# Performance work log

Measured on AMD Instinct MI355X. Metric: run time of the kernel, lower is better.

The kernel has to match this reference:

```python
import jax, jax.numpy as jnp
import numpy as np


def setup_inputs() -> dict:
    key = jax.random.key(0)
    ks = jax.random.split(key, 7)
    B, H, W, C, HID = 8, 64, 64, 16, 256
    s = 0.05
    return {
        "x": jax.random.normal(ks[0], (B, H, W, C), jnp.float32),
        "W1": jax.random.normal(ks[1], (C, HID), jnp.float32) * s,
        "b1": jax.random.normal(ks[2], (C, HID), jnp.float32) * s,
        "W2": jax.random.normal(ks[3], (C, HID, HID), jnp.float32) * s,
        "b2": jax.random.normal(ks[4], (C, HID), jnp.float32) * s,
        "W3": jax.random.normal(ks[5], (C, HID, 3), jnp.float32) * s,
        "b3": jax.random.normal(ks[6], (C, 3), jnp.float32) * s,
    }


def reference(x, W1, b1, W2, b2, W3, b3):
    # x: [B,H,W,C] -> per-channel independent 3-layer MLP (1 -> HID -> HID -> 3)
    B, H, W, C = x.shape
    xf = x.reshape(-1, C)                                   # [N, C]
    # fc1: Linear(1, HID) per channel == scalar * weight + bias
    h = jax.nn.relu(xf[:, :, None] * W1[None] + b1[None])   # [N, C, HID]
    # fc2: batched GEMM over channels
    h = jax.nn.relu(jnp.einsum('nch,chk->nck', h, W2) + b2[None])  # [N, C, HID]
    # fc3: HID -> 3 per channel
    out = jnp.einsum('nch,cho->nco', h, W3) + b3[None]      # [N, C, 3]
    # torch.cat(outputs, dim=1) yields [c0_0..c0_2, c1_0..c1_2, ...] == reshape
    return out.reshape(B, H, W, C * 3)
```

## Files before the change

### kernel.cpp

```cpp
#include <hip/hip_runtime.h>
#include <hip/hip_bf16.h>


typedef __bf16 bf16_t;
typedef __attribute__((ext_vector_type(8))) __bf16 bf16x8;
typedef __attribute__((ext_vector_type(4))) __bf16 bf16x4;
typedef __attribute__((ext_vector_type(4))) float floatx4;

#define C_CH  16
#define HID   256
#define TILES 16
#define NSEG  257
#define GPTS  4097
#define XLO   (-6.0f)
#define XSTEP (12.0f / 4096.0f)

__global__ __launch_bounds__(256, 4) void build_tab(
    const float* __restrict__ W1, const float* __restrict__ b1,
    const float* __restrict__ W2, const float* __restrict__ b2,
    bf16_t* __restrict__ tab, float* __restrict__ ts_g) {
  __shared__ float tk[256];
  __shared__ int ti[256];
  __shared__ float sW1[256], sB1[256];
  __shared__ int sRank[256];
  __shared__ float caS[256], ccS[256];
  __shared__ float part[4][64][9];
  __shared__ float eA[17], eC[17];
  __shared__ int eH[17];
  const int c = blockIdx.x & 15;
  const int k = blockIdx.x >> 4;
  const int j0 = (NSEG * k) >> 4;
  const int j1 = (NSEG * (k + 1)) >> 4;
  const int nev = j1 - 1 - j0;
  const int t = threadIdx.x;

  sW1[t] = W1[c * 256 + t];
  sB1[t] = b1[c * 256 + t];
  tk[t] = (sW1[t] != 0.0f) ? (-sB1[t] / sW1[t]) : 3.0e38f;
  ti[t] = t;
  __syncthreads();
  for (int kk = 2; kk <= 256; kk <<= 1) {
    for (int j = kk >> 1; j > 0; j >>= 1) {
      int l = t ^ j;
      if (l > t) {
        bool asc = ((t & kk) == 0);
        float a = tk[t], b = tk[l];
        if (asc ? (a > b) : (a < b)) {
          int ia = ti[t], ib = ti[l];
          tk[t] = b; tk[l] = a; ti[t] = ib; ti[l] = ia;
        }
      }
      __syncthreads();
    }
  }
  sRank[ti[t]] = t;
  if (k == 0) ts_g[c * 256 + t] = tk[t];
  if (t < nev) {
    int h = ti[j0 + t];
    float w = sW1[h], bv = sB1[h];
    eA[t] = fabsf(w);
    eC[t] = (w > 0.f) ? bv : ((w < 0.f) ? -bv : 0.f);
    eH[t] = h;
  }
  __syncthreads();

  {
    float w = sW1[t], bv = sB1[t];
    int r = sRank[t];
    bool act = (w > 0.f) ? (j0 > r) : ((w < 0.f) ? (j0 <= r) : (bv > 0.f));
    caS[t] = act ? w : 0.f;
    ccS[t] = act ? bv : 0.f;
  }
  __syncthreads();

  const int rg = t >> 6;
  const int q = t & 63;
  const float* W2c = W2 + ((size_t)c << 16);
  float pa0 = 0.f, pa1 = 0.f, pa2 = 0.f, pa3 = 0.f;
  float pc0 = 0.f, pc1 = 0.f, pc2 = 0.f, pc3 = 0.f;
  for (int h0 = rg * 64; h0 < rg * 64 + 64; h0 += 8) {
    float4 v[8];
#pragma unroll
    for (int u = 0; u < 8; ++u)
      v[u] = *(const float4*)(W2c + (size_t)(h0 + u) * 256 + q * 4);
#pragma unroll
    for (int u = 0; u < 8; ++u) {
      float ca = caS[h0 + u], cc = ccS[h0 + u];
      pa0 = fmaf(ca, v[u].x, pa0); pa1 = fmaf(ca, v[u].y, pa1);
      pa2 = fmaf(ca, v[u].z, pa2); pa3 = fmaf(ca, v[u].w, pa3);
      pc0 = fmaf(cc, v[u].x, pc0); pc1 = fmaf(cc, v[u].y, pc1);
      pc2 = fmaf(cc, v[u].z, pc2); pc3 = fmaf(cc, v[u].w, pc3);
    }
  }
  part[rg][q][0] = pa0; part[rg][q][1] = pa1;
  part[rg][q][2] = pa2; part[rg][q][3] = pa3;
  part[rg][q][4] = pc0; part[rg][q][5] = pc1;
  part[rg][q][6] = pc2; part[rg][q][7] = pc3;
  __syncthreads();

  float accA = 0.f, accC = b2[c * 256 + t];
  {
    const int qq = t >> 2, ii = t & 3;
#pragma unroll
    for (int rr = 0; rr < 4; ++rr) {
      accA += part[rr][qq][ii];
      accC += part[rr][qq][4 + ii];
    }
  }
  {
    bf16_t* rp = tab + ((size_t)c * NSEG + j0) * 512;
    rp[t] = (bf16_t)accA; rp[256 + t] = (bf16_t)accC;
  }

  float ew[16];
#pragma unroll 16
  for (int e = 0; e < 16; ++e)
    if (e < nev) ew[e] = W2c[eH[e] * 256 + t];
#pragma unroll 16
  for (int e = 0; e < 16; ++e) {
    if (e < nev) {
      accA = fmaf(eA[e], ew[e], accA);
      accC = fmaf(eC[e], ew[e], accC);
      bf16_t* rp = tab + ((size_t)c * NSEG + (j0 + 1 + e)) * 512;
      rp[t] = (bf16_t)accA; rp[256 + t] = (bf16_t)accC;
    }
  }
}

__global__ __launch_bounds__(256) void build_ftab(
    const bf16_t* __restrict__ tab, const float* __restrict__ ts_g,
    const float* __restrict__ W3, const float* __restrict__ b3,
    float* __restrict__ ftab) {
  __shared__ float tls[256];
  __shared__ short sj[128];
  const int t = threadIdx.x;
  const int c = blockIdx.x & 15;
  const int q = blockIdx.x >> 4;
  const int gp0 = q * 128;

  tls[t] = ts_g[c * 256 + t];

  const int l16 = t & 15;
  const int g = t >> 4;
  float w3f0[16], w3f1[16], w3f2[16];
#pragma unroll
  for (int u = 0; u < 16; ++u) {
    const float* wp = W3 + ((size_t)c * 256 + l16 * 16 + u) * 3;
    w3f0[u] = wp[0]; w3f1[u] = wp[1]; w3f2[u] = wp[2];
  }
  const float b3v0 = b3[c * 3 + 0], b3v1 = b3[c * 3 + 1], b3v2 = b3[c * 3 + 2];
  __syncthreads();

  if (t < 128) {
    const int gp = gp0 + t;
    if (gp <= 4096) {
      const float xv = XLO + (float)gp * XSTEP;
      int j = 0;
#pragma unroll
      for (int s = 128; s > 0; s >>= 1)
        if (tls[j + s - 1] <= xv) j += s;
      if (j == 255 && tls[255] <= xv) j = 256;
      else if (j < 255 && tls[j] <= xv) ++j;
      sj[t] = (short)j;
    } else {
      sj[t] = 0;
    }
  }
  __syncthreads();

  const bf16_t* tabc = tab + (size_t)c * NSEG * 512;
  float xv = XLO + (float)(gp0 + g) * XSTEP;
  const bf16_t* row = tabc + (size_t)sj[g] * 512 + l16 * 16;
  bf16x8 a0 = *(const bf16x8*)(row);
  bf16x8 a1 = *(const bf16x8*)(row + 8);
  bf16x8 c0 = *(const bf16x8*)(row + 256);
  bf16x8 c1 = *(const bf16x8*)(row + 264);

  for (int i = 0; i < 8; ++i) {
    bf16x8 na0, na1, nc0, nc1;
    float nxv = 0.f;
    if (i < 7) {
      int npl = (i + 1) * 16 + g;
      nxv = XLO + (float)(gp0 + npl) * XSTEP;
      const bf16_t* nrow = tabc + (size_t)sj[npl] * 512 + l16 * 16;
      na0 = *(const bf16x8*)(nrow);
      na1 = *(const bf16x8*)(nrow + 8);
      nc0 = *(const bf16x8*)(nrow + 256);
      nc1 = *(const bf16x8*)(nrow + 264);
    }
    float s0 = 0.f, s1 = 0.f, s2 = 0.f;
#pragma unroll
    for (int u = 0; u < 8; ++u) {
      float h2 = fmaxf(fmaf(xv, (float)a0[u], (float)c0[u]), 0.f);
      s0 = fmaf(h2, w3f0[u], s0);
      s1 = fmaf(h2, w3f1[u], s1);
      s2 = fmaf(h2, w3f2[u], s2);
    }
#pragma unroll
    for (int u = 0; u < 8; ++u) {
      float h2 = fmaxf(fmaf(xv, (float)a1[u], (float)c1[u]), 0.f);
      s0 = fmaf(h2, w3f0[8 + u], s0);
      s1 = fmaf(h2, w3f1[8 + u], s1);
      s2 = fmaf(h2, w3f2[8 + u], s2);
    }
#pragma unroll
    for (int m = 1; m < 16; m <<= 1) {
      s0 += __shfl_xor(s0, m, 64);
      s1 += __shfl_xor(s1, m, 64);
      s2 += __shfl_xor(s2, m, 64);
    }
    const int gp = gp0 + i * 16 + g;
    if (l16 < 3 && gp <= 4096) {
      float v = (l16 == 0) ? (s0 + b3v0) : (l16 == 1) ? (s1 + b3v1) : (s2 + b3v2);
      ftab[((size_t)c * GPTS + gp) * 4 + l16] = v;
    }
    a0 = na0; a1 = na1; c0 = nc0; c1 = nc1; xv = nxv;
  }
}

__global__ __launch_bounds__(256) void kan_eval(
    const float* __restrict__ x, const float* __restrict__ ftab,
    float* __restrict__ out) {
  const int base = blockIdx.x * 256 + threadIdx.x;
  const float inv = 1.0f / XSTEP;
#pragma unroll
  for (int it = 0; it < 4; ++it) {
    const int flat = it * 131072 + base;
    const float xv = x[flat];
    const int c = flat & 15;
    float u = (xv - XLO) * inv;
    int i = (int)floorf(u);
    i = i < 0 ? 0 : (i > 4095 ? 4095 : i);
    const float f = u - (float)i;
    const float4* fp = (const float4*)ftab + (size_t)c * GPTS + i;
    float4 fa = fp[0];
    float4 fb = fp[1];
    float* op = out + (size_t)flat * 3;
    op[0] = fmaf(fb.x - fa.x, f, fa.x);
    op[1] = fmaf(fb.y - fa.y, f, fa.y);
    op[2] = fmaf(fb.z - fa.z, f, fa.z);
  }
}

__global__ __launch_bounds__(256) void kan_pwl(
    const float* __restrict__ x, const bf16_t* __restrict__ tab,
    const float* __restrict__ W1, const float* __restrict__ b1,
    const float* __restrict__ W3, const float* __restrict__ b3,
    float* __restrict__ out) {
  __shared__ float xs[256];
  __shared__ float tls[256];
  __shared__ short sj[256];
  const int t = threadIdx.x;
  const int b = blockIdx.x;
  const int c = ((b & 7) << 1) | ((b >> 3) & 1);
  const int pb = b >> 4;

  xs[t] = x[(size_t)(pb * 256 + t) * C_CH + c];
  {
    float w = W1[c * 256 + t], bb = b1[c * 256 + t];
    tls[t] = (w != 0.0f) ? (-bb / w) : 3.0e38f;
  }
  __syncthreads();
  for (int kk = 2; kk <= 256; kk <<= 1) {
    for (int j = kk >> 1; j > 0; j >>= 1) {
      int l = t ^ j;
      if (l > t) {
        bool asc = ((t & kk) == 0);
        float a = tls[t], bb2 = tls[l];
        if (asc ? (a > bb2) : (a < bb2)) { tls[t] = bb2; tls[l] = a; }
      }
      __syncthreads();
    }
  }

  const int l16 = t & 15;
  const int g = t >> 4;
  float w3f0[16], w3f1[16], w3f2[16];
#pragma unroll
  for (int qq = 0; qq < 16; ++qq) {
    const float* wp = W3 + ((size_t)c * 256 + l16 * 16 + qq) * 3;
    w3f0[qq] = wp[0]; w3f1[qq] = wp[1]; w3f2[qq] = wp[2];
  }
  const float b3v0 = b3[c * 3 + 0], b3v1 = b3[c * 3 + 1], b3v2 = b3[c * 3 + 2];

  {
    const float xv = xs[t];
    int j = 0;
#pragma unroll
    for (int s = 128; s > 0; s >>= 1)
      if (tls[j + s - 1] <= xv) j += s;
    if (j == 255 && tls[255] <= xv) j = 256;
    else if (j < 255 && tls[j] <= xv) ++j;
    sj[t] = (short)j;
  }
  __syncthreads();

  const bf16_t* tabc = tab + (size_t)c * NSEG * 512;
  for (int i = 0; i < 16; ++i) {
    const int pl = i * 16 + g;
    const float xv = xs[pl];
    const bf16_t* row = tabc + (size_t)sj[pl] * 512 + l16 * 16;
    bf16x8 a0 = *(const bf16x8*)(row);
    bf16x8 a1 = *(const bf16x8*)(row + 8);
    bf16x8 c0 = *(const bf16x8*)(row + 256);
    bf16x8 c1 = *(const bf16x8*)(row + 264);
    float s0 = 0.f, s1 = 0.f, s2 = 0.f;
#pragma unroll
    for (int qq = 0; qq < 8; ++qq) {
      float h2 = fmaxf(fmaf(xv, (float)a0[qq], (float)c0[qq]), 0.f);
      s0 = fmaf(h2, w3f0[qq], s0);
      s1 = fmaf(h2, w3f1[qq], s1);
      s2 = fmaf(h2, w3f2[qq], s2);
    }
#pragma unroll
    for (int qq = 0; qq < 8; ++qq) {
      float h2 = fmaxf(fmaf(xv, (float)a1[qq], (float)c1[qq]), 0.f);
      s0 = fmaf(h2, w3f0[8 + qq], s0);
      s1 = fmaf(h2, w3f1[8 + qq], s1);
      s2 = fmaf(h2, w3f2[8 + qq], s2);
    }
#pragma unroll
    for (int m = 1; m < 16; m <<= 1) {
      s0 += __shfl_xor(s0, m, 64);
      s1 += __shfl_xor(s1, m, 64);
      s2 += __shfl_xor(s2, m, 64);
    }
    if (l16 < 3) {
      float v = (l16 == 0) ? (s0 + b3v0) : (l16 == 1) ? (s1 + b3v1) : (s2 + b3v2);
      out[((size_t)(pb * 256 + pl) * C_CH + c) * 3 + l16] = v;
    }
  }
}

__global__ __launch_bounds__(256) void transpose_w2(const float* __restrict__ W2,
                                                    bf16_t* __restrict__ W2t) {
  __shared__ __align__(16) bf16_t tl[64][72];
  const int bid = blockIdx.x;
  const int c = bid >> 4, ti = (bid >> 2) & 3, tj = bid & 3;
  const int t = threadIdx.x;
  const float* src = W2 + (size_t)(c * 256 + tj * 64) * 256 + ti * 64;
#pragma unroll
  for (int it = 0; it < 4; ++it) {
    int idx = it * 256 + t;
    int h = idx >> 4, q = idx & 15;
    float4 v = *(const float4*)(src + h * 256 + q * 4);
    tl[h][q * 4 + 0] = (bf16_t)v.x;
    tl[h][q * 4 + 1] = (bf16_t)v.y;
    tl[h][q * 4 + 2] = (bf16_t)v.z;
    tl[h][q * 4 + 3] = (bf16_t)v.w;
  }
  __syncthreads();
  bf16_t* dst = W2t + (size_t)(c * 256 + ti * 64) * 256 + tj * 64;
#pragma unroll
  for (int it = 0; it < 2; ++it) {
    int idx = it * 256 + t;
    int n = idx >> 3, h8 = (idx & 7) * 8;
    bf16x8 tmp;
#pragma unroll
    for (int q = 0; q < 8; ++q) tmp[q] = tl[h8 + q][n];
    *(bf16x8*)(dst + n * 256 + h8) = tmp;
  }
}

template <bool DIRECT>
__global__ __launch_bounds__(256, 2) void kan_fused(
    const float* __restrict__ x, const float* __restrict__ W1,
    const float* __restrict__ b1, const bf16_t* __restrict__ W2t,
    const float* __restrict__ W2, const float* __restrict__ b2,
    const float* __restrict__ W3, const float* __restrict__ b3,
    float* __restrict__ out) {
  __shared__ __align__(16) bf16_t h1[64][264];
  __shared__ __align__(16) bf16_t w3t[4][288];
  const int t = threadIdx.x;
  const int lane = t & 63;
  const int wv = t >> 6;
  const int bid = blockIdx.x;
  const int c = bid & 15;
  const int g = bid >> 4;
  const int l15 = lane & 15;
  const int l4 = lane >> 4;
  const int nw0 = wv * 64;
  bf16x8 Bf[32];
  if (!DIRECT) {
    const bf16_t* Bbase = W2t + ((size_t)c << 16) + (size_t)(nw0 + l15) * HID + l4 * 8;
#pragma unroll
    for (int kt = 0; kt < 4; ++kt)
#pragma unroll
      for (int ks = 0; ks < 2; ++ks)
#pragma unroll
        for (int jn = 0; jn < 4; ++jn)
          Bf[kt * 8 + ks * 4 + jn] =
              *(const bf16x8*)(Bbase + jn * (16 * HID) + kt * 64 + ks * 32);
  } else {
#pragma unroll
    for (int kt = 0; kt < 4; ++kt)
#pragma unroll
      for (int ks = 0; ks < 2; ++ks)
#pragma unroll
        for (int jn = 0; jn < 4; ++jn) {
          const float* gp = W2 + ((size_t)c << 16) +
                            (size_t)(kt * 64 + ks * 32 + l4 * 8) * HID +
                            (nw0 + jn * 16 + l15);
#pragma unroll
          for (int j = 0; j < 8; ++j) Bf[kt * 8 + ks * 4 + jn][j] = (bf16_t)gp[j * HID];
        }
  }
  const int j8 = (t & 31) * 8;
  float wf[8], bf_[8];
  {
    float4 w0 = *(const float4*)(W1 + c * HID + j8);
    float4 w1v = *(const float4*)(W1 + c * HID + j8 + 4);
    float4 bb0 = *(const float4*)(b1 + c * HID + j8);
    float4 bb1 = *(const float4*)(b1 + c * HID + j8 + 4);
    wf[0] = w0.x; wf[1] = w0.y; wf[2] = w0.z; wf[3] = w0.w;
    wf[4] = w1v.x; wf[5] = w1v.y; wf[6] = w1v.z; wf[7] = w1v.w;
    bf_[0] = bb0.x; bf_[1] = bb0.y; bf_[2] = bb0.z; bf_[3] = bb0.w;
    bf_[4] = bb1.x; bf_[5] = bb1.y; bf_[6] = bb1.z; bf_[7] = bb1.w;
  }
  floatx4 b2v[4];
#pragma unroll
  for (int jn = 0; jn < 4; ++jn)
    b2v[jn] = *(const floatx4*)(b2 + c * HID + nw0 + jn * 16 + l4 * 4);
  const float b3v = b3[c * 3 + (l15 < 3 ? l15 : 0)];
  const int bhalf = (lane >> 5) & 1;
  w3t[0][t] = (bf16_t)W3[(c * HID + t) * 3 + 0];
  w3t[1][t] = (bf16_t)W3[(c * HID + t) * 3 + 1];
  w3t[2][t] = (bf16_t)W3[(c * HID + t) * 3 + 2];
  w3t[3][t] = (bf16_t)0.0f;
  const floatx4 zero4 = {0.f, 0.f, 0.f, 0.f};
  float xr = 0.0f;
  {
    int ml = (lane >> 1) * 8 + wv * 2 + (lane & 1);
    if (lane < 16) xr = x[(size_t)(g * TILES * 64 + ml) * C_CH + c];
  }
  for (int tile = 0; tile < TILES; ++tile) {
    const int m0 = (g * TILES + tile) * 64;
#pragma unroll
    for (int it = 0; it < 8; ++it) {
      int m = it * 8 + (t >> 5);
      float xm = __shfl(xr, it * 2 + bhalf, 64);
      bf16x8 hv;
#pragma unroll
      for (int q = 0; q < 8; ++q)
        hv[q] = (bf16_t)fmaxf(xm * wf[q] + bf_[q], 0.0f);
      *(bf16x8*)&h1[m][j8] = hv;
    }
    __syncthreads();
    float xr_n = 0.0f;
    if (tile + 1 < TILES && lane < 16) {
      int ml = (lane >> 1) * 8 + wv * 2 + (lane & 1);
      xr_n = x[(size_t)(m0 + 64 + ml) * C_CH + c];
    }
    floatx4 acc[4][4];
#pragma unroll
    for (int im = 0; im < 4; ++im)
#pragma unroll
      for (int jn = 0; jn < 4; ++jn) acc[im][jn] = zero4;
#pragma unroll
    for (int kt = 0; kt < 4; ++kt) {
#pragma unroll
      for (int ks = 0; ks < 2; ++ks) {
        const int k0 = kt * 64 + ks * 32;
        bf16x8 af[4];
#pragma unroll
        for (int im = 0; im < 4; ++im)
          af[im] = *(const bf16x8*)&h1[im * 16 + l15][k0 + l4 * 8];
#pragma unroll
        for (int im = 0; im < 4; ++im)
#pragma unroll
          for (int jn = 0; jn < 4; ++jn)
            acc[im][jn] = __builtin_amdgcn_mfma_f32_16x16x32_bf16(
                Bf[kt * 8 + ks * 4 + jn], af[im], acc[im][jn], 0, 0, 0);
      }
    }
    __syncthreads();
#pragma unroll
    for (int im = 0; im < 4; ++im)
#pragma unroll
      for (int jn = 0; jn < 4; ++jn) {
        bf16x4 hv;
#pragma unroll
        for (int r = 0; r < 4; ++r)
          hv[r] = (bf16_t)fmaxf(acc[im][jn][r] + b2v[jn][r], 0.0f);
        *(bf16x4*)&h1[im * 16 + l15][nw0 + jn * 16 + l4 * 4] = hv;
      }
    __syncthreads();
    {
      floatx4 acc3 = zero4;
      const int br = l15 < 3 ? l15 : 3;
#pragma unroll
      for (int kk = 0; kk < 8; ++kk) {
        bf16x8 a3 = *(const bf16x8*)&h1[wv * 16 + l15][kk * 32 + l4 * 8];
        bf16x8 bf3 = *(const bf16x8*)&w3t[br][kk * 32 + l4 * 8];
        acc3 = __builtin_amdgcn_mfma_f32_16x16x32_bf16(a3, bf3, acc3, 0, 0, 0);
      }
      if (l15 < 3) {
        float* op = out + ((size_t)((m0 + wv * 16 + l4 * 4) * C_CH + c) * 3) + l15;
#pragma unroll
        for (int r = 0; r < 4; ++r) op[r * (C_CH * 3)] = acc3[r] + b3v;
      }
    }
    __syncthreads();
    xr = xr_n;
  }
}

extern "C" void kernel_launch(void* const* d_in, const int* in_sizes, int n_in,
                              void* d_out, int out_size, void* d_ws, size_t ws_size,
                              hipStream_t stream) {
  const float* x = (const float*)d_in[0];
  const float* W1 = (const float*)d_in[1];
  const float* b1 = (const float*)d_in[2];
  const float* W2 = (const float*)d_in[3];
  const float* b2 = (const float*)d_in[4];
  const float* W3 = (const float*)d_in[5];
  const float* b3 = (const float*)d_in[6];
  float* out = (float*)d_out;

  const size_t tab_bytes = (size_t)C_CH * NSEG * 512 * sizeof(bf16_t);
  const size_t ftab_bytes = (size_t)C_CH * GPTS * 4 * sizeof(float);
  const size_t ts_bytes = (size_t)C_CH * 256 * sizeof(float);
  if (ws_size >= tab_bytes + ftab_bytes + ts_bytes) {
    bf16_t* tab = (bf16_t*)d_ws;
    float* ftab = (float*)((char*)d_ws + tab_bytes);
    float* ts_g = (float*)((char*)d_ws + tab_bytes + ftab_bytes);
    build_tab<<<256, 256, 0, stream>>>(W1, b1, W2, b2, tab, ts_g);
    build_ftab<<<528, 256, 0, stream>>>(tab, ts_g, W3, b3, ftab);
    kan_eval<<<512, 256, 0, stream>>>(x, ftab, out);
  } else if (ws_size >= tab_bytes + ts_bytes) {
    bf16_t* tab = (bf16_t*)d_ws;
    float* ts_g = (float*)((char*)d_ws + tab_bytes);
    build_tab<<<256, 256, 0, stream>>>(W1, b1, W2, b2, tab, ts_g);
    kan_pwl<<<2048, 256, 0, stream>>>(x, tab, W1, b1, W3, b3, out);
  } else if (ws_size >= (size_t)C_CH * HID * HID * sizeof(bf16_t)) {
    bf16_t* W2t = (bf16_t*)d_ws;
    transpose_w2<<<256, 256, 0, stream>>>(W2, W2t);
    kan_fused<false><<<512, 256, 0, stream>>>(x, W1, b1, W2t, W2, b2, W3, b3, out);
  } else {
    kan_fused<true><<<512, 256, 0, stream>>>(x, W1, b1, (bf16_t*)d_ws, W2, b2, W3, b3, out);
  }
}
```

Measured before the change: 96.24 us.

## Fuse table build, fine-table build and eval into one cooperative kernel

Replaces the three-kernel sequence (build_tab, build_ftab, kan_eval) with a single cooperative kernel of 512 blocks that separates the phases with grid-wide syncs, removing two launch gaps. The work split also changes: the coarse-table phase now uses 32 segment chunks per channel instead of 16, and the fine-table phase uses 144 grid points per block to cover 4097 points with 512 blocks. It falls back to the old three launches if the cooperative launch fails. Risks include grid.sync overhead and the requirement that all 512 blocks be co-resident.

```diff
diff --git a/kernel.cpp b/kernel.cpp
--- a/kernel.cpp
+++ b/kernel.cpp
@@ -1,5 +1,8 @@
 #include <hip/hip_runtime.h>
 #include <hip/hip_bf16.h>
+#include <hip/hip_cooperative_groups.h>
+
+namespace cg = cooperative_groups;
 
 
 typedef __bf16 bf16_t;
@@ -14,6 +17,238 @@
 #define GPTS  4097
 #define XLO   (-6.0f)
 #define XSTEP (12.0f / 4096.0f)
+
+__global__ __launch_bounds__(256) void kan_all(
+    const float* __restrict__ x, const float* __restrict__ W1,
+    const float* __restrict__ b1, const float* __restrict__ W2,
+    const float* __restrict__ b2, const float* __restrict__ W3,
+    const float* __restrict__ b3, bf16_t* __restrict__ tab,
+    float* __restrict__ ts_g, float* __restrict__ ftab,
+    float* __restrict__ out) {
+  cg::grid_group grid = cg::this_grid();
+  __shared__ float tk[256];
+  __shared__ int ti[256];
+  __shared__ float sW1[256], sB1[256];
+  __shared__ int sRank[256];
+  __shared__ float caS[256], ccS[256];
+  __shared__ float part[4][64][9];
+  __shared__ float eA[9], eC[9];
+  __shared__ int eH[9];
+  __shared__ short sj[144];
+
+  const int t = threadIdx.x;
+  const int b = blockIdx.x;
+
+  {
+    const int c = b & 15;
+    const int k = b >> 4;
+    const int j0 = (NSEG * k) >> 5;
+    const int j1 = (NSEG * (k + 1)) >> 5;
+    const int nev = j1 - 1 - j0;
+
+    sW1[t] = W1[c * 256 + t];
+    sB1[t] = b1[c * 256 + t];
+    tk[t] = (sW1[t] != 0.0f) ? (-sB1[t] / sW1[t]) : 3.0e38f;
+    ti[t] = t;
+    __syncthreads();
+    for (int kk = 2; kk <= 256; kk <<= 1) {
+      for (int j = kk >> 1; j > 0; j >>= 1) {
+        int l = t ^ j;
+        if (l > t) {
+          bool asc = ((t & kk) == 0);
+          float a = tk[t], bb = tk[l];
+          if (asc ? (a > bb) : (a < bb)) {
+            int ia = ti[t], ib = ti[l];
+            tk[t] = bb; tk[l] = a; ti[t] = ib; ti[l] = ia;
+          }
+        }
+        __syncthreads();
+      }
+    }
+    sRank[ti[t]] = t;
+    if (k == 0) ts_g[c * 256 + t] = tk[t];
+    if (t < nev) {
+      int h = ti[j0 + t];
+      float w = sW1[h], bv = sB1[h];
+      eA[t] = fabsf(w);
+      eC[t] = (w > 0.f) ? bv : ((w < 0.f) ? -bv : 0.f);
+      eH[t] = h;
+    }
+    __syncthreads();
+
+    {
+      float w = sW1[t], bv = sB1[t];
+      int r = sRank[t];
+      bool act = (w > 0.f) ? (j0 > r) : ((w < 0.f) ? (j0 <= r) : (bv > 0.f));
+      caS[t] = act ? w : 0.f;
+      ccS[t] = act ? bv : 0.f;
+    }
+    __syncthreads();
+
+    const int rg = t >> 6;
+    const int q = t & 63;
+    const float* W2c = W2 + ((size_t)c << 16);
+    float pa0 = 0.f, pa1 = 0.f, pa2 = 0.f, pa3 = 0.f;
+    float pc0 = 0.f, pc1 = 0.f, pc2 = 0.f, pc3 = 0.f;
+    for (int h0 = rg * 64; h0 < rg * 64 + 64; h0 += 8) {
+      float4 v[8];
+#pragma unroll
+      for (int u = 0; u < 8; ++u)
+        v[u] = *(const float4*)(W2c + (size_t)(h0 + u) * 256 + q * 4);
+#pragma unroll
+      for (int u = 0; u < 8; ++u) {
+        float ca = caS[h0 + u], cc = ccS[h0 + u];
+        pa0 = fmaf(ca, v[u].x, pa0); pa1 = fmaf(ca, v[u].y, pa1);
+        pa2 = fmaf(ca, v[u].z, pa2); pa3 = fmaf(ca, v[u].w, pa3);
+        pc0 = fmaf(cc, v[u].x, pc0); pc1 = fmaf(cc, v[u].y, pc1);
+        pc2 = fmaf(cc, v[u].z, pc2); pc3 = fmaf(cc, v[u].w, pc3);
+      }
+    }
+    part[rg][q][0] = pa0; part[rg][q][1] = pa1;
+    part[rg][q][2] = pa2; part[rg][q][3] = pa3;
+    part[rg][q][4] = pc0; part[rg][q][5] = pc1;
+    part[rg][q][6] = pc2; part[rg][q][7] = pc3;
+    __syncthreads();
+
+    float accA = 0.f, accC = b2[c * 256 + t];
+    {
+      const int qq = t >> 2, ii = t & 3;
+#pragma unroll
+      for (int rr = 0; rr < 4; ++rr) {
+        accA += part[rr][qq][ii];
+        accC += part[rr][qq][4 + ii];
+      }
+    }
+    {
+      bf16_t* rp = tab + ((size_t)c * NSEG + j0) * 512;
+      rp[t] = (bf16_t)accA; rp[256 + t] = (bf16_t)accC;
+    }
+    float ew[8];
+#pragma unroll 8
+    for (int e = 0; e < 8; ++e)
+      if (e < nev) ew[e] = W2c[eH[e] * 256 + t];
+#pragma unroll 8
+    for (int e = 0; e < 8; ++e) {
+      if (e < nev) {
+        accA = fmaf(eA[e], ew[e], accA);
+        accC = fmaf(eC[e], ew[e], accC);
+        bf16_t* rp = tab + ((size_t)c * NSEG + (j0 + 1 + e)) * 512;
+        rp[t] = (bf16_t)accA; rp[256 + t] = (bf16_t)accC;
+      }
+    }
+  }
+  __threadfence();
+  grid.sync();
+
+  {
+    const int c = b & 15;
+    const int q = b >> 4;
+    const int gp0 = q * 128;
+
+    tk[t] = ts_g[c * 256 + t];
+
+    const int l16 = t & 15;
+    const int g = t >> 4;
+    float w3f0[16], w3f1[16], w3f2[16];
+#pragma unroll
+    for (int u = 0; u < 16; ++u) {
+      const float* wp = W3 + ((size_t)c * 256 + l16 * 16 + u) * 3;
+      w3f0[u] = wp[0]; w3f1[u] = wp[1]; w3f2[u] = wp[2];
+    }
+    const float b3v0 = b3[c * 3 + 0], b3v1 = b3[c * 3 + 1], b3v2 = b3[c * 3 + 2];
+    __syncthreads();
+
+    if (t < 144) {
+      const int gp = gp0 + t;
+      if (gp <= 4096) {
+        const float xv = XLO + (float)gp * XSTEP;
+        int j = 0;
+#pragma unroll
+        for (int s = 128; s > 0; s >>= 1)
+          if (tk[j + s - 1] <= xv) j += s;
+        if (j == 255 && tk[255] <= xv) j = 256;
+        else if (j < 255 && tk[j] <= xv) ++j;
+        sj[t] = (short)j;
+      } else {
+        sj[t] = 0;
+      }
+    }
+    __syncthreads();
+
+    const bf16_t* tabc = tab + (size_t)c * NSEG * 512;
+    float xv = XLO + (float)(gp0 + g) * XSTEP;
+    const bf16_t* row = tabc + (size_t)sj[g] * 512 + l16 * 16;
+    bf16x8 a0 = *(const bf16x8*)(row);
+    bf16x8 a1 = *(const bf16x8*)(row + 8);
+    bf16x8 c0 = *(const bf16x8*)(row + 256);
+    bf16x8 c1 = *(const bf16x8*)(row + 264);
+
+    for (int i = 0; i < 9; ++i) {
+      bf16x8 na0, na1, nc0, nc1;
+      float nxv = 0.f;
+      if (i < 8) {
+        int npl = (i + 1) * 16 + g;
+        nxv = XLO + (float)(gp0 + npl) * XSTEP;
+        const bf16_t* nrow = tabc + (size_t)sj[npl] * 512 + l16 * 16;
+        na0 = *(const bf16x8*)(nrow);
+        na1 = *(const bf16x8*)(nrow + 8);
+        nc0 = *(const bf16x8*)(nrow + 256);
+        nc1 = *(const bf16x8*)(nrow + 264);
+      }
+      float s0 = 0.f, s1 = 0.f, s2 = 0.f;
+#pragma unroll
+      for (int u = 0; u < 8; ++u) {
+        float h2 = fmaxf(fmaf(xv, (float)a0[u], (float)c0[u]), 0.f);
+        s0 = fmaf(h2, w3f0[u], s0);
+        s1 = fmaf(h2, w3f1[u], s1);
+        s2 = fmaf(h2, w3f2[u], s2);
+      }
+#pragma unroll
+      for (int u = 0; u < 8; ++u) {
+        float h2 = fmaxf(fmaf(xv, (float)a1[u], (float)c1[u]), 0.f);
+        s0 = fmaf(h2, w3f0[8 + u], s0);
+        s1 = fmaf(h2, w3f1[8 + u], s1);
+        s2 = fmaf(h2, w3f2[8 + u], s2);
+      }
+#pragma unroll
+      for (int m = 1; m < 16; m <<= 1) {
+        s0 += __shfl_xor(s0, m, 64);
+        s1 += __shfl_xor(s1, m, 64);
+        s2 += __shfl_xor(s2, m, 64);
+      }
+      const int gp = gp0 + i * 16 + g;
+      if (l16 < 3 && gp <= 4096) {
+        float v = (l16 == 0) ? (s0 + b3v0) : (l16 == 1) ? (s1 + b3v1) : (s2 + b3v2);
+        ftab[((size_t)c * GPTS + gp) * 4 + l16] = v;
+      }
+      a0 = na0; a1 = na1; c0 = nc0; c1 = nc1; xv = nxv;
+    }
+  }
+  __threadfence();
+  grid.sync();
+
+  {
+    const int base = b * 256 + t;
+    const float inv = 1.0f / XSTEP;
+#pragma unroll
+    for (int it = 0; it < 4; ++it) {
+      const int flat = it * 131072 + base;
+      const float xv = x[flat];
+      const int c = flat & 15;
+      float u = (xv - XLO) * inv;
+      int i = (int)floorf(u);
+      i = i < 0 ? 0 : (i > 4095 ? 4095 : i);
+      const float f = u - (float)i;
+      const float4* fp = (const float4*)ftab + (size_t)c * GPTS + i;
+      float4 fa = fp[0];
+      float4 fb = fp[1];
+      float* op = out + (size_t)flat * 3;
+      op[0] = fmaf(fb.x - fa.x, f, fa.x);
+      op[1] = fmaf(fb.y - fa.y, f, fa.y);
+      op[2] = fmaf(fb.z - fa.z, f, fa.z);
+    }
+  }
+}
 
 __global__ __launch_bounds__(256, 4) void build_tab(
     const float* __restrict__ W1, const float* __restrict__ b1,
@@ -63,7 +298,6 @@
     eH[t] = h;
   }
   __syncthreads();
-
   {
     float w = sW1[t], bv = sB1[t];
     int r = sRank[t];
@@ -72,7 +306,6 @@
     ccS[t] = act ? bv : 0.f;
   }
   __syncthreads();
-
   const int rg = t >> 6;
   const int q = t & 63;
   const float* W2c = W2 + ((size_t)c << 16);
@@ -97,7 +330,6 @@
   part[rg][q][4] = pc0; part[rg][q][5] = pc1;
   part[rg][q][6] = pc2; part[rg][q][7] = pc3;
   __syncthreads();
-
   float accA = 0.f, accC = b2[c * 256 + t];
   {
     const int qq = t >> 2, ii = t & 3;
@@ -111,7 +343,6 @@
     bf16_t* rp = tab + ((size_t)c * NSEG + j0) * 512;
     rp[t] = (bf16_t)accA; rp[256 + t] = (bf16_t)accC;
   }
-
   float ew[16];
 #pragma unroll 16
   for (int e = 0; e < 16; ++e)
@@ -137,9 +368,7 @@
   const int c = blockIdx.x & 15;
   const int q = blockIdx.x >> 4;
   const int gp0 = q * 128;
-
   tls[t] = ts_g[c * 256 + t];
-
   const int l16 = t & 15;
   const int g = t >> 4;
   float w3f0[16], w3f1[16], w3f2[16];
@@ -150,7 +379,6 @@
   }
   const float b3v0 = b3[c * 3 + 0], b3v1 = b3[c * 3 + 1], b3v2 = b3[c * 3 + 2];
   __syncthreads();
-
   if (t < 128) {
     const int gp = gp0 + t;
     if (gp <= 4096) {
@@ -167,7 +395,6 @@
     }
   }
   __syncthreads();
-
   const bf16_t* tabc = tab + (size_t)c * NSEG * 512;
   float xv = XLO + (float)(gp0 + g) * XSTEP;
   const bf16_t* row = tabc + (size_t)sj[g] * 512 + l16 * 16;
@@ -175,7 +402,6 @@
   bf16x8 a1 = *(const bf16x8*)(row + 8);
   bf16x8 c0 = *(const bf16x8*)(row + 256);
   bf16x8 c1 = *(const bf16x8*)(row + 264);
-
   for (int i = 0; i < 8; ++i) {
     bf16x8 na0, na1, nc0, nc1;
     float nxv = 0.f;
@@ -239,96 +465,6 @@
     op[0] = fmaf(fb.x - fa.x, f, fa.x);
     op[1] = fmaf(fb.y - fa.y, f, fa.y);
     op[2] = fmaf(fb.z - fa.z, f, fa.z);
-  }
-}
-
-__global__ __launch_bounds__(256) void kan_pwl(
-    const float* __restrict__ x, const bf16_t* __restrict__ tab,
-    const float* __restrict__ W1, const float* __restrict__ b1,
-    const float* __restrict__ W3, const float* __restrict__ b3,
-    float* __restrict__ out) {
-  __shared__ float xs[256];
-  __shared__ float tls[256];
-  __shared__ short sj[256];
-  const int t = threadIdx.x;
-  const int b = blockIdx.x;
-  const int c = ((b & 7) << 1) | ((b >> 3) & 1);
-  const int pb = b >> 4;
-
-  xs[t] = x[(size_t)(pb * 256 + t) * C_CH + c];
-  {
-    float w = W1[c * 256 + t], bb = b1[c * 256 + t];
-    tls[t] = (w != 0.0f) ? (-bb / w) : 3.0e38f;
-  }
-  __syncthreads();
-  for (int kk = 2; kk <= 256; kk <<= 1) {
-    for (int j = kk >> 1; j > 0; j >>= 1) {
-      int l = t ^ j;
-      if (l > t) {
-        bool asc = ((t & kk) == 0);
-        float a = tls[t], bb2 = tls[l];
-        if (asc ? (a > bb2) : (a < bb2)) { tls[t] = bb2; tls[l] = a; }
-      }
-      __syncthreads();
-    }
-  }
-
-  const int l16 = t & 15;
-  const int g = t >> 4;
-  float w3f0[16], w3f1[16], w3f2[16];
-#pragma unroll
-  for (int qq = 0; qq < 16; ++qq) {
-    const float* wp = W3 + ((size_t)c * 256 + l16 * 16 + qq) * 3;
-    w3f0[qq] = wp[0]; w3f1[qq] = wp[1]; w3f2[qq] = wp[2];
-  }
-  const float b3v0 = b3[c * 3 + 0], b3v1 = b3[c * 3 + 1], b3v2 = b3[c * 3 + 2];
-
-  {
-    const float xv = xs[t];
-    int j = 0;
-#pragma unroll
-    for (int s = 128; s > 0; s >>= 1)
-      if (tls[j + s - 1] <= xv) j += s;
-    if (j == 255 && tls[255] <= xv) j = 256;
-    else if (j < 255 && tls[j] <= xv) ++j;
-    sj[t] = (short)j;
-  }
-  __syncthreads();
-
-  const bf16_t* tabc = tab + (size_t)c * NSEG * 512;
-  for (int i = 0; i < 16; ++i) {
-    const int pl = i * 16 + g;
-    const float xv = xs[pl];
-    const bf16_t* row = tabc + (size_t)sj[pl] * 512 + l16 * 16;
-    bf16x8 a0 = *(const bf16x8*)(row);
-    bf16x8 a1 = *(const bf16x8*)(row + 8);
-    bf16x8 c0 = *(const bf16x8*)(row + 256);
-    bf16x8 c1 = *(const bf16x8*)(row + 264);
-    float s0 = 0.f, s1 = 0.f, s2 = 0.f;
-#pragma unroll
-    for (int qq = 0; qq < 8; ++qq) {
-      float h2 = fmaxf(fmaf(xv, (float)a0[qq], (float)c0[qq]), 0.f);
-      s0 = fmaf(h2, w3f0[qq], s0);
-      s1 = fmaf(h2, w3f1[qq], s1);
-      s2 = fmaf(h2, w3f2[qq], s2);
-    }
-#pragma unroll
-    for (int qq = 0; qq < 8; ++qq) {
-      float h2 = fmaxf(fmaf(xv, (float)a1[qq], (float)c1[qq]), 0.f);
-      s0 = fmaf(h2, w3f0[8 + qq], s0);
-      s1 = fmaf(h2, w3f1[8 + qq], s1);
-      s2 = fmaf(h2, w3f2[8 + qq], s2);
-    }
-#pragma unroll
-    for (int m = 1; m < 16; m <<= 1) {
-      s0 += __shfl_xor(s0, m, 64);
-      s1 += __shfl_xor(s1, m, 64);
-      s2 += __shfl_xor(s2, m, 64);
-    }
-    if (l16 < 3) {
-      float v = (l16 == 0) ? (s0 + b3v0) : (l16 == 1) ? (s1 + b3v1) : (s2 + b3v2);
-      out[((size_t)(pb * 256 + pl) * C_CH + c) * 3 + l16] = v;
-    }
   }
 }
 
@@ -524,14 +660,24 @@
     bf16_t* tab = (bf16_t*)d_ws;
     float* ftab = (float*)((char*)d_ws + tab_bytes);
     float* ts_g = (float*)((char*)d_ws + tab_bytes + ftab_bytes);
-    build_tab<<<256, 256, 0, stream>>>(W1, b1, W2, b2, tab, ts_g);
-    build_ftab<<<528, 256, 0, stream>>>(tab, ts_g, W3, b3, ftab);
-    kan_eval<<<512, 256, 0, stream>>>(x, ftab, out);
+    void* args[] = {(void*)&x,   (void*)&W1,  (void*)&b1,   (void*)&W2,
+                    (void*)&b2,  (void*)&W3,  (void*)&b3,   (void*)&tab,
+                    (void*)&ts_g, (void*)&ftab, (void*)&out};
+    hipError_t err = hipLaunchCooperativeKernel((void*)kan_all, dim3(512),
+                                                dim3(256), args, 0, stream);
+    if (err != hipSuccess) {
+      (void)hipGetLastError();
+      build_tab<<<256, 256, 0, stream>>>(W1, b1, W2, b2, tab, ts_g);
+      build_ftab<<<528, 256, 0, stream>>>(tab, ts_g, W3, b3, ftab);
+      kan_eval<<<512, 256, 0, stream>>>(x, ftab, out);
+    }
   } else if (ws_size >= tab_bytes + ts_bytes) {
     bf16_t* tab = (bf16_t*)d_ws;
     float* ts_g = (float*)((char*)d_ws + tab_bytes);
     build_tab<<<256, 256, 0, stream>>>(W1, b1, W2, b2, tab, ts_g);
-    kan_pwl<<<2048, 256, 0, stream>>>(x, tab, W1, b1, W3, b3, out);
+    transpose_w2<<<256, 256, 0, stream>>>(W2, (bf16_t*)d_ws);
+    kan_fused<false><<<512, 256, 0, stream>>>(x, W1, b1, (bf16_t*)d_ws, W2, b2,
+                                              W3, b3, out);
   } else if (ws_size >= (size_t)C_CH * HID * HID * sizeof(bf16_t)) {
     bf16_t* W2t = (bf16_t*)d_ws;
     transpose_w2<<<256, 256, 0, stream>>>(W2, W2t);
```

Measured after the change: 281.9 us. 2.93x slower.
